# Kernel optimization log

Measured on AMD Instinct MI355X. Metric: run time of the kernel, lower is better.

## Reference

```python
import jax, jax.numpy as jnp
import numpy as np

V, D, T_MAX, H, L = 32000, 1024, 1024, 16, 8
HD = D // H
DFF = 4 * D
EPS = 1e-5


def _pos_encoding(T, d_model, dtype=jnp.float32):
    pos = jnp.arange(T, dtype=jnp.float32)[:, None]                      # [T,1]
    div = jnp.exp(jnp.arange(0, d_model, 2, dtype=jnp.float32) * (-jnp.log(10000.0) / d_model))
    pe = jnp.zeros((T, d_model), dtype=jnp.float32)
    pe = pe.at[:, 0::2].set(jnp.sin(pos * div))
    pe = pe.at[:, 1::2].set(jnp.cos(pos * div))
    return pe.astype(dtype)


def _layernorm(x, g, b):
    mu = jnp.mean(x, axis=-1, keepdims=True)
    var = jnp.mean(jnp.square(x - mu), axis=-1, keepdims=True)
    return (x - mu) * jax.lax.rsqrt(var + EPS) * g + b


def setup_inputs() -> dict:
    key = jax.random.key(0)
    ks = jax.random.split(key, 9)
    s = 0.02
    return {
        "idx": jax.random.randint(ks[0], (2, 1024), 0, V),
        "embed": jax.random.normal(ks[1], (V, D), jnp.float32) * s,
        "Wqkv": jax.random.normal(ks[2], (L, D, 3 * D), jnp.float32) * s,
        "Wproj": jax.random.normal(ks[3], (L, D, D), jnp.float32) * s,
        "bproj": jnp.zeros((L, D), jnp.float32),
        "ln1_g": jnp.ones((L, D), jnp.float32),
        "ln1_b": jnp.zeros((L, D), jnp.float32),
        "ln2_g": jnp.ones((L, D), jnp.float32),
        "ln2_b": jnp.zeros((L, D), jnp.float32),
        "W1": jax.random.normal(ks[4], (L, D, DFF), jnp.float32) * s,
        "b1": jnp.zeros((L, DFF), jnp.float32),
        "W2": jax.random.normal(ks[5], (L, DFF, D), jnp.float32) * s,
        "b2": jnp.zeros((L, D), jnp.float32),
        "lnf_g": jnp.ones((D,), jnp.float32),
        "lnf_b": jnp.zeros((D,), jnp.float32),
        "Whead": jax.random.normal(ks[6], (D, V), jnp.float32) * s,
    }


def _attn(x, Wqkv, Wproj, bproj):
    B, T, C = x.shape
    qkv = (x @ Wqkv).reshape(B, T, 3, H, HD)
    q, k, v = [jnp.transpose(qkv[:, :, i], (0, 2, 1, 3)) for i in range(3)]  # [B,H,T,HD]
    scores = jnp.einsum('bhqd,bhkd->bhqk', q, k) * (HD ** -0.5)
    mask = jnp.tril(jnp.ones((T, T), dtype=bool))
    scores = jnp.where(mask, scores, -jnp.inf)
    w = jax.nn.softmax(scores, axis=-1)
    out = jnp.einsum('bhqk,bhkd->bhqd', w, v)
    out = jnp.transpose(out, (0, 2, 1, 3)).reshape(B, T, C)
    return out @ Wproj + bproj


def reference(idx, embed, Wqkv, Wproj, bproj, ln1_g, ln1_b, ln2_g, ln2_b,
              W1, b1, W2, b2, lnf_g, lnf_b, Whead):
    idx = idx[:, :T_MAX]
    T = idx.shape[1]
    x = embed[idx] + _pos_encoding(T, D)[None]          # [B,T,D]
    for l in range(L):
        x = x + _attn(_layernorm(x, ln1_g[l], ln1_b[l]), Wqkv[l], Wproj[l], bproj[l])
        h = _layernorm(x, ln2_g[l], ln2_b[l])
        x = x + jax.nn.relu(h @ W1[l] + b1[l]) @ W2[l] + b2[l]
    x = _layernorm(x, lnf_g, lnf_b)
    return x @ Whead                                     # [B,T,V]
```

## Files before the change

### kernel.cpp

```cpp
#include <hip/hip_runtime.h>
#include <cstddef>

#define DM    1024
#define TSEQ  1024
#define NB    2
#define NHEAD 16
#define HDIM  64
#define NLAYER 8
#define DFFN  4096
#define NVOC  32000
#define NROWS (NB*TSEQ)

typedef __attribute__((ext_vector_type(8))) short short8;
typedef __attribute__((ext_vector_type(4))) float f32x4;

static __device__ __forceinline__ unsigned short f2bf(float f) {
    union { float f; unsigned int u; } v; v.f = f;
    unsigned int r = v.u + 0x7FFF + ((v.u >> 16) & 1);
    return (unsigned short)(r >> 16);
}

static __device__ __forceinline__ void gload_lds16(const void* g, void* l) {
    __builtin_amdgcn_global_load_lds(
        (const __attribute__((address_space(1))) unsigned int*)g,
        (__attribute__((address_space(3))) unsigned int*)l, 16, 0, 0);
}

__global__ __launch_bounds__(256)
void embed_pos_k(const int* __restrict__ idx, const float* __restrict__ embed,
                 float* __restrict__ x)
{
    int row = blockIdx.x;
    int t   = row & (TSEQ - 1);
    int tid = threadIdx.x;
    int token = idx[row];
    const float* er = embed + (size_t)token * DM;
    float* xr = x + (size_t)row * DM;
    const float neg_ln1e4_over_d = -9.210340371976184f / (float)DM;
    for (int i = tid; i < DM; i += 256) {
        int half = i >> 1;
        float div = expf((float)(2 * half) * neg_ln1e4_over_d);
        float ang = (float)t * div;
        float pe = (i & 1) ? cosf(ang) : sinf(ang);
        xr[i] = er[i] + pe;
    }
}

__global__ __launch_bounds__(256)
void layernorm_k(const float* __restrict__ x, const float* __restrict__ g,
                 const float* __restrict__ b, unsigned short* __restrict__ y)
{
    int row = blockIdx.x;
    int tid = threadIdx.x;
    const float* xr = x + (size_t)row * DM;
    unsigned short* yr = y + (size_t)row * DM;
    float vals[4];
    float s = 0.f;
    #pragma unroll
    for (int i = 0; i < 4; ++i) { vals[i] = xr[tid + 256 * i]; s += vals[i]; }
    __shared__ float red[256];
    red[tid] = s; __syncthreads();
    for (int st = 128; st > 0; st >>= 1) {
        if (tid < st) red[tid] += red[tid + st];
        __syncthreads();
    }
    float mu = red[0] * (1.f / DM);
    __syncthreads();
    float v = 0.f;
    #pragma unroll
    for (int i = 0; i < 4; ++i) { float d = vals[i] - mu; v += d * d; }
    red[tid] = v; __syncthreads();
    for (int st = 128; st > 0; st >>= 1) {
        if (tid < st) red[tid] += red[tid + st];
        __syncthreads();
    }
    float rstd = rsqrtf(red[0] * (1.f / DM) + 1e-5f);
    #pragma unroll
    for (int i = 0; i < 4; ++i) {
        int c = tid + 256 * i;
        yr[c] = f2bf((vals[i] - mu) * rstd * g[c] + b[c]);
    }
}

__global__ __launch_bounds__(256)
void convt_k(const float* __restrict__ src, unsigned short* __restrict__ dst,
             int K, int N)
{
    __shared__ __align__(16) unsigned short T[64][72];
    const int tid = threadIdx.x;
    const int n0 = blockIdx.x * 64, k0 = blockIdx.y * 64;
    const float* s = src + (size_t)blockIdx.z * K * N;
    unsigned short* d = dst + (size_t)blockIdx.z * K * N;
    #pragma unroll
    for (int q = 0; q < 4; ++q) {
        int f4 = tid + q * 256;
        int kk = f4 >> 4, nn = (f4 & 15) * 4;
        float4 v = *(const float4*)(s + (size_t)(k0 + kk) * N + n0 + nn);
        int swz = ((nn >> 2) & 7) << 3;
        T[nn + 0][kk ^ swz] = f2bf(v.x);
        T[nn + 1][kk ^ swz] = f2bf(v.y);
        T[nn + 2][kk ^ swz] = f2bf(v.z);
        T[nn + 3][kk ^ swz] = f2bf(v.w);
    }
    __syncthreads();
    #pragma unroll
    for (int q = 0; q < 2; ++q) {
        int s8 = tid + q * 256;
        int nn = s8 >> 3, kc = (s8 & 7) * 8;
        int swz = ((nn >> 2) & 7) << 3;
        *(short8*)(d + (size_t)(n0 + nn) * K + k0 + kc) =
            *(const short8*)&T[nn][kc ^ swz];
    }
}

template<int BM, bool OUT_BF16>
__global__ __launch_bounds__(256)
void gemm_tn(const unsigned short* __restrict__ A, const unsigned short* __restrict__ BT,
             const float* __restrict__ bias, const float* __restrict__ residual,
             void* __restrict__ Cout, int M, int N, int K, int KS, int relu)
{
    constexpr int FR = BM / 32;
    constexpr int RPW = BM / 4;
    constexpr int NI = BM / 64;
    __shared__ __align__(16) unsigned short As[2][BM][32];
    __shared__ __align__(16) unsigned short Bs[2][BM][32];

    const int tid = threadIdx.x;
    const int lane = tid & 63;
    const int w = tid >> 6;
    const int wr = w >> 1, wc = w & 1;
    const int l16 = lane & 15, g = lane >> 4;

    const int nby = M / BM;
    const int nwg = (N / BM) * nby;
    const int cpx = nwg >> 3;
    const int bid = blockIdx.x;
    const int sbid = (bid & 7) * cpx + (bid >> 3);
    const int row0 = (sbid % nby) * BM;
    const int col0 = (sbid / nby) * BM;

    const int srow = w * RPW + (lane >> 2);
    const int scol = (lane & 3) * 8;

    const unsigned short* ga = A  + (size_t)(row0 + srow) * KS + (size_t)blockIdx.y * K + scol;
    const unsigned short* gb = BT + (size_t)(col0 + srow) * KS + (size_t)blockIdx.y * K + scol;

    f32x4 acc[FR][FR] = {};

    #pragma unroll
    for (int i = 0; i < NI; ++i) {
        gload_lds16(ga + (size_t)(i * 16) * KS, &As[0][srow + i * 16][scol]);
        gload_lds16(gb + (size_t)(i * 16) * KS, &Bs[0][srow + i * 16][scol]);
    }
    __syncthreads();

    int cur = 0;
    for (int k0 = 0; k0 < K; k0 += 32) {
        if (k0 + 32 < K) {
            #pragma unroll
            for (int i = 0; i < NI; ++i) {
                gload_lds16(ga + k0 + 32 + (size_t)(i * 16) * KS, &As[cur ^ 1][srow + i * 16][scol]);
                gload_lds16(gb + k0 + 32 + (size_t)(i * 16) * KS, &Bs[cur ^ 1][srow + i * 16][scol]);
            }
        }
        short8 af[FR], bf[FR];
        #pragma unroll
        for (int i = 0; i < FR; ++i)
            af[i] = *(const short8*)&As[cur][wr * (BM / 2) + i * 16 + l16][g * 8];
        #pragma unroll
        for (int j = 0; j < FR; ++j)
            bf[j] = *(const short8*)&Bs[cur][wc * (BM / 2) + j * 16 + l16][g * 8];
        #pragma unroll
        for (int i = 0; i < FR; ++i)
            #pragma unroll
            for (int j = 0; j < FR; ++j)
                acc[i][j] = __builtin_amdgcn_mfma_f32_16x16x32_bf16(af[i], bf[j], acc[i][j], 0, 0, 0);
        __syncthreads();
        cur ^= 1;
    }

    float* Cf = (float*)Cout + (size_t)blockIdx.y * M * N;
    #pragma unroll
    for (int i = 0; i < FR; ++i) {
        #pragma unroll
        for (int j = 0; j < FR; ++j) {
            #pragma unroll
            for (int r = 0; r < 4; ++r) {
                int row = row0 + wr * (BM / 2) + i * 16 + g * 4 + r;
                int col = col0 + wc * (BM / 2) + j * 16 + l16;
                float v = acc[i][j][r];
                if (bias)     v += bias[col];
                if (residual) v += residual[(size_t)row * N + col];
                if (relu)     v = fmaxf(v, 0.f);
                if (OUT_BF16) ((unsigned short*)Cout)[(size_t)row * N + col] = f2bf(v);
                else          Cf[(size_t)row * N + col] = v;
            }
        }
    }
}

__global__ __launch_bounds__(256)
void reduce_sk(const float* __restrict__ P, int nsplit, const float* __restrict__ bias,
               const float* __restrict__ Xres, float* __restrict__ X, int Ncols)
{
    const size_t i4 = (size_t)blockIdx.x * 256 + threadIdx.x;
    const int col4 = (int)(i4 & (Ncols / 4 - 1)) * 4;
    float4 v = *(const float4*)(Xres + i4 * 4);
    float4 bb = *(const float4*)(bias + col4);
    v.x += bb.x; v.y += bb.y; v.z += bb.z; v.w += bb.w;
    const size_t tot4 = (size_t)NROWS * Ncols / 4;
    for (int s = 0; s < nsplit; ++s) {
        float4 p = *(const float4*)(P + (s * tot4 + i4) * 4);
        v.x += p.x; v.y += p.y; v.z += p.z; v.w += p.w;
    }
    *(float4*)(X + i4 * 4) = v;
}

__global__ __launch_bounds__(256)
void attn_flash_k(const unsigned short* __restrict__ qkv, unsigned short* __restrict__ out)
{
    __shared__ unsigned short Ks[64][72];
    __shared__ unsigned short Vt[64][72];
    __shared__ unsigned short Ps[4][16][72];

    const int tid = threadIdx.x;
    const int lane = tid & 63;
    const int w = tid >> 6;
    const int l16 = lane & 15, g = lane >> 4;
    const int h = blockIdx.y;
    const int b = blockIdx.z;

    const size_t rstr = 3 * DM;
    const unsigned short* base = qkv + (size_t)b * TSEQ * rstr + h * HDIM;

    const int krow0 = tid >> 3, kcol = (tid & 7) * 8;
    const int vkv = tid & 63, vdg = tid >> 6;

    short8 kreg0, kreg1, vreg0, vreg1;

    #pragma unroll
    for (int pass = 0; pass < 2; ++pass) {
        const int qb = pass ? (15 - (int)blockIdx.x) : (int)blockIdx.x;
        const int q0 = qb * 64;
        const int nt = qb + 1;

        const int qrow_w = q0 + w * 16 + l16;
        short8 aq0 = *(const short8*)(base + (size_t)qrow_w * rstr + g * 8);
        short8 aq1 = *(const short8*)(base + (size_t)qrow_w * rstr + 32 + g * 8);

        f32x4 acc_o[4] = {};
        float m_r[4] = {-INFINITY, -INFINITY, -INFINITY, -INFINITY};
        float l_r[4] = {};

        {
            const unsigned short* kb = base + DM;
            kreg0 = *(const short8*)(kb + (size_t)krow0 * rstr + kcol);
            kreg1 = *(const short8*)(kb + (size_t)(32 + krow0) * rstr + kcol);
            const unsigned short* vsrc = base + (size_t)vkv * rstr + 2 * DM + vdg * 16;
            vreg0 = *(const short8*)vsrc;
            vreg1 = *(const short8*)(vsrc + 8);
        }

        for (int t = 0; t < nt; ++t) {
            *(short8*)&Ks[krow0][kcol] = kreg0;
            *(short8*)&Ks[32 + krow0][kcol] = kreg1;
            #pragma unroll
            for (int j = 0; j < 8; ++j) Vt[vdg * 16 + j][vkv] = (unsigned short)vreg0[j];
            #pragma unroll
            for (int j = 0; j < 8; ++j) Vt[vdg * 16 + 8 + j][vkv] = (unsigned short)vreg1[j];
            __syncthreads();

            if (t + 1 < nt) {
                const int kv0 = (t + 1) * 64;
                const unsigned short* kb = base + (size_t)kv0 * rstr + DM;
                kreg0 = *(const short8*)(kb + (size_t)krow0 * rstr + kcol);
                kreg1 = *(const short8*)(kb + (size_t)(32 + krow0) * rstr + kcol);
                const unsigned short* vsrc = base + (size_t)(kv0 + vkv) * rstr + 2 * DM + vdg * 16;
                vreg0 = *(const short8*)vsrc;
                vreg1 = *(const short8*)(vsrc + 8);
            }

            const int kv0 = t * 64;
            f32x4 acc_s[4] = {};
            #pragma unroll
            for (int ks = 0; ks < 4; ++ks) {
                short8 bk0 = *(const short8*)&Ks[ks * 16 + l16][g * 8];
                short8 bk1 = *(const short8*)&Ks[ks * 16 + l16][32 + g * 8];
                acc_s[ks] = __builtin_amdgcn_mfma_f32_16x16x32_bf16(aq0, bk0, acc_s[ks], 0, 0, 0);
                acc_s[ks] = __builtin_amdgcn_mfma_f32_16x16x32_bf16(aq1, bk1, acc_s[ks], 0, 0, 0);
            }
            const bool need_mask = (kv0 + 63 > q0 + w * 16);
            float alpha[4];
            #pragma unroll
            for (int r = 0; r < 4; ++r) {
                const int q_abs = q0 + w * 16 + g * 4 + r;
                float s[4];
                #pragma unroll
                for (int ks = 0; ks < 4; ++ks) {
                    s[ks] = acc_s[ks][r] * 0.125f;
                    if (need_mask && (kv0 + ks * 16 + l16 > q_abs)) s[ks] = -INFINITY;
                }
                float pm = fmaxf(fmaxf(s[0], s[1]), fmaxf(s[2], s[3]));
                #pragma unroll
                for (int msk = 1; msk <= 8; msk <<= 1)
                    pm = fmaxf(pm, __shfl_xor(pm, msk));
                float mnew = fmaxf(m_r[r], pm);
                alpha[r] = __expf(m_r[r] - mnew);
                m_r[r] = mnew;
                float p[4], psum = 0.f;
                #pragma unroll
                for (int ks = 0; ks < 4; ++ks) {
                    p[ks] = (s[ks] == -INFINITY) ? 0.f : __expf(s[ks] - mnew);
                    psum += p[ks];
                }
                #pragma unroll
                for (int msk = 1; msk <= 8; msk <<= 1)
                    psum += __shfl_xor(psum, msk);
                l_r[r] = l_r[r] * alpha[r] + psum;
                #pragma unroll
                for (int ks = 0; ks < 4; ++ks)
                    Ps[w][g * 4 + r][ks * 16 + l16] = f2bf(p[ks]);
            }
            #pragma unroll
            for (int ds = 0; ds < 4; ++ds)
                #pragma unroll
                for (int r = 0; r < 4; ++r)
                    acc_o[ds][r] *= alpha[r];
            short8 ap0 = *(const short8*)&Ps[w][l16][g * 8];
            short8 ap1 = *(const short8*)&Ps[w][l16][32 + g * 8];
            #pragma unroll
            for (int ds = 0; ds < 4; ++ds) {
                short8 bv0 = *(const short8*)&Vt[ds * 16 + l16][g * 8];
                short8 bv1 = *(const short8*)&Vt[ds * 16 + l16][32 + g * 8];
                acc_o[ds] = __builtin_amdgcn_mfma_f32_16x16x32_bf16(ap0, bv0, acc_o[ds], 0, 0, 0);
                acc_o[ds] = __builtin_amdgcn_mfma_f32_16x16x32_bf16(ap1, bv1, acc_o[ds], 0, 0, 0);
            }
            __syncthreads();
        }

        #pragma unroll
        for (int ds = 0; ds < 4; ++ds)
            #pragma unroll
            for (int r = 0; r < 4; ++r) {
                int row = q0 + w * 16 + g * 4 + r;
                out[((size_t)b * TSEQ + row) * DM + h * HDIM + ds * 16 + l16] =
                    f2bf(acc_o[ds][r] * (1.f / l_r[r]));
            }
    }
}

extern "C" void kernel_launch(void* const* d_in, const int* in_sizes, int n_in,
                              void* d_out, int out_size, void* d_ws, size_t ws_size,
                              hipStream_t stream)
{
    const int*   idx    = (const int*)  d_in[0];
    const float* embed  = (const float*)d_in[1];
    const float* Wqkv   = (const float*)d_in[2];
    const float* Wproj  = (const float*)d_in[3];
    const float* bproj  = (const float*)d_in[4];
    const float* ln1_g  = (const float*)d_in[5];
    const float* ln1_b  = (const float*)d_in[6];
    const float* ln2_g  = (const float*)d_in[7];
    const float* ln2_b  = (const float*)d_in[8];
    const float* W1     = (const float*)d_in[9];
    const float* b1     = (const float*)d_in[10];
    const float* W2     = (const float*)d_in[11];
    const float* b2     = (const float*)d_in[12];
    const float* lnf_g  = (const float*)d_in[13];
    const float* lnf_b  = (const float*)d_in[14];
    const float* Whead  = (const float*)d_in[15];
    float* out = (float*)d_out;

    float* X = (float*)d_ws;
    float* PK = X + (size_t)NROWS * DM;
    unsigned short* u = (unsigned short*)(PK + (size_t)4 * NROWS * DM);
    unsigned short* XN     = u;  u += (size_t)NROWS * DM;
    unsigned short* QKVb   = u;  u += (size_t)NROWS * 3 * DM;
    unsigned short* ATT    = u;  u += (size_t)NROWS * DM;
    unsigned short* FFH    = u;  u += (size_t)NROWS * DFFN;
    unsigned short* WqkvT  = u;  u += (size_t)NLAYER * 3 * DM * DM;
    unsigned short* WprojT = u;  u += (size_t)NLAYER * DM * DM;
    unsigned short* W1T    = u;  u += (size_t)NLAYER * DFFN * DM;
    unsigned short* W2T    = u;  u += (size_t)NLAYER * DM * DFFN;
    unsigned short* WheadT = u;  u += (size_t)NVOC * DM;

    convt_k<<<dim3(3 * DM / 64, DM / 64, NLAYER), 256, 0, stream>>>(Wqkv,  WqkvT,  DM,   3 * DM);
    convt_k<<<dim3(DM / 64,     DM / 64, NLAYER), 256, 0, stream>>>(Wproj, WprojT, DM,   DM);
    convt_k<<<dim3(DFFN / 64,   DM / 64, NLAYER), 256, 0, stream>>>(W1,    W1T,    DM,   DFFN);
    convt_k<<<dim3(DM / 64,   DFFN / 64, NLAYER), 256, 0, stream>>>(W2,    W2T,    DFFN, DM);
    convt_k<<<dim3(NVOC / 64,   DM / 64, 1),      256, 0, stream>>>(Whead, WheadT, DM,   NVOC);

    embed_pos_k<<<NROWS, 256, 0, stream>>>(idx, embed, X);

    const int nred = (NROWS * DM / 4) / 256;

    for (int l = 0; l < NLAYER; ++l) {
        const unsigned short* wqkvT_l  = WqkvT  + (size_t)l * 3 * DM * DM;
        const unsigned short* wprojT_l = WprojT + (size_t)l * DM * DM;
        const unsigned short* w1T_l    = W1T    + (size_t)l * DFFN * DM;
        const unsigned short* w2T_l    = W2T    + (size_t)l * DM * DFFN;
        const float* bproj_l = bproj + (size_t)l * DM;
        const float* b1_l = b1 + (size_t)l * DFFN;
        const float* b2_l = b2 + (size_t)l * DM;

        layernorm_k<<<NROWS, 256, 0, stream>>>(X, ln1_g + (size_t)l * DM,
                                               ln1_b + (size_t)l * DM, XN);
        {
            int nwg = (NROWS / 128) * (3 * DM / 128);
            gemm_tn<128, true><<<nwg, 256, 0, stream>>>(XN, wqkvT_l, nullptr, nullptr,
                                                        QKVb, NROWS, 3 * DM, DM, DM, 0);
        }
        {
            dim3 grid(TSEQ / 128, NHEAD, NB);
            attn_flash_k<<<grid, 256, 0, stream>>>(QKVb, ATT);
        }
        {
            dim3 grid((NROWS / 128) * (DM / 128), 2);
            gemm_tn<128, false><<<grid, 256, 0, stream>>>(ATT, wprojT_l, nullptr, nullptr,
                                                          PK, NROWS, DM, 512, DM, 0);
            reduce_sk<<<nred, 256, 0, stream>>>(PK, 2, bproj_l, X, X, DM);
        }
        layernorm_k<<<NROWS, 256, 0, stream>>>(X, ln2_g + (size_t)l * DM,
                                               ln2_b + (size_t)l * DM, XN);
        {
            int nwg = (NROWS / 128) * (DFFN / 128);
            gemm_tn<128, true><<<nwg, 256, 0, stream>>>(XN, w1T_l, b1_l, nullptr,
                                                        FFH, NROWS, DFFN, DM, DM, 1);
        }
        {
            dim3 grid((NROWS / 128) * (DM / 128), 4);
            gemm_tn<128, false><<<grid, 256, 0, stream>>>(FFH, w2T_l, nullptr, nullptr,
                                                          PK, NROWS, DM, 1024, DFFN, 0);
            reduce_sk<<<nred, 256, 0, stream>>>(PK, 4, b2_l, X, X, DM);
        }
    }

    layernorm_k<<<NROWS, 256, 0, stream>>>(X, lnf_g, lnf_b, XN);
    {
        int nwg = (NROWS / 128) * (NVOC / 128);
        gemm_tn<128, false><<<nwg, 256, 0, stream>>>(XN, WheadT, nullptr, nullptr,
                                                     out, NROWS, NVOC, DM, DM, 0);
    }
}
```

Before: 1.905 ms.

## Fuse split-K reduction with layernorm and swizzle GEMM LDS layout

Replaces the separate split-K reduce and layernorm kernels with one row-wise kernel. It sums the partials, adds the bias and residual, writes X, then computes the next layernorm into the bf16 buffer. This removes a kernel launch and a full re-read of X per residual step. It also XOR-swizzles the GEMM LDS column slots, on both the global-to-LDS writes and the fragment reads, to reduce bank conflicts. The risk is a wrong swizzle mapping between the write and read sides.

```diff
diff --git a/kernel.cpp b/kernel.cpp
--- a/kernel.cpp
+++ b/kernel.cpp
@@ -83,6 +83,52 @@
 }
 
 __global__ __launch_bounds__(256)
+void reduce_ln_k(const float* __restrict__ P, int nsplit, const float* __restrict__ bias,
+                 float* __restrict__ X, const float* __restrict__ g,
+                 const float* __restrict__ b, unsigned short* __restrict__ XN)
+{
+    const int row = blockIdx.x;
+    const int tid = threadIdx.x;
+    const size_t off4 = (size_t)row * 256 + tid;
+    const size_t tot4 = (size_t)NROWS * 256;
+
+    float4 v = *((const float4*)X + off4);
+    float4 bb = *((const float4*)bias + tid);
+    v.x += bb.x; v.y += bb.y; v.z += bb.z; v.w += bb.w;
+    for (int s = 0; s < nsplit; ++s) {
+        float4 p = *((const float4*)P + s * tot4 + off4);
+        v.x += p.x; v.y += p.y; v.z += p.z; v.w += p.w;
+    }
+    *((float4*)X + off4) = v;
+
+    __shared__ float red[256];
+    red[tid] = v.x + v.y + v.z + v.w;
+    __syncthreads();
+    for (int st = 128; st > 0; st >>= 1) {
+        if (tid < st) red[tid] += red[tid + st];
+        __syncthreads();
+    }
+    float mu = red[0] * (1.f / DM);
+    __syncthreads();
+    float4 d = make_float4(v.x - mu, v.y - mu, v.z - mu, v.w - mu);
+    red[tid] = d.x * d.x + d.y * d.y + d.z * d.z + d.w * d.w;
+    __syncthreads();
+    for (int st = 128; st > 0; st >>= 1) {
+        if (tid < st) red[tid] += red[tid + st];
+        __syncthreads();
+    }
+    float rstd = rsqrtf(red[0] * (1.f / DM) + 1e-5f);
+    float4 gg = *((const float4*)g + tid);
+    float4 bbn = *((const float4*)b + tid);
+    unsigned short o[4];
+    o[0] = f2bf(d.x * rstd * gg.x + bbn.x);
+    o[1] = f2bf(d.y * rstd * gg.y + bbn.y);
+    o[2] = f2bf(d.z * rstd * gg.z + bbn.z);
+    o[3] = f2bf(d.w * rstd * gg.w + bbn.w);
+    *(ushort4*)(XN + (size_t)row * DM + tid * 4) = *(ushort4*)o;
+}
+
+__global__ __launch_bounds__(256)
 void convt_k(const float* __restrict__ src, unsigned short* __restrict__ dst,
              int K, int N)
 {
@@ -140,7 +186,8 @@
     const int col0 = (sbid / nby) * BM;
 
     const int srow = w * RPW + (lane >> 2);
-    const int scol = (lane & 3) * 8;
+    const int scol = (((lane & 3) ^ ((lane >> 3) & 3)) << 3);
+    const int rslot = ((g ^ ((l16 >> 1) & 3)) << 3);
 
     const unsigned short* ga = A  + (size_t)(row0 + srow) * KS + (size_t)blockIdx.y * K + scol;
     const unsigned short* gb = BT + (size_t)(col0 + srow) * KS + (size_t)blockIdx.y * K + scol;
@@ -149,8 +196,8 @@
 
     #pragma unroll
     for (int i = 0; i < NI; ++i) {
-        gload_lds16(ga + (size_t)(i * 16) * KS, &As[0][srow + i * 16][scol]);
-        gload_lds16(gb + (size_t)(i * 16) * KS, &Bs[0][srow + i * 16][scol]);
+        gload_lds16(ga + (size_t)(i * 16) * KS, &As[0][srow + i * 16][(lane & 3) << 3]);
+        gload_lds16(gb + (size_t)(i * 16) * KS, &Bs[0][srow + i * 16][(lane & 3) << 3]);
     }
     __syncthreads();
 
@@ -159,17 +206,17 @@
         if (k0 + 32 < K) {
             #pragma unroll
             for (int i = 0; i < NI; ++i) {
-                gload_lds16(ga + k0 + 32 + (size_t)(i * 16) * KS, &As[cur ^ 1][srow + i * 16][scol]);
-                gload_lds16(gb + k0 + 32 + (size_t)(i * 16) * KS, &Bs[cur ^ 1][srow + i * 16][scol]);
+                gload_lds16(ga + k0 + 32 + (size_t)(i * 16) * KS, &As[cur ^ 1][srow + i * 16][(lane & 3) << 3]);
+                gload_lds16(gb + k0 + 32 + (size_t)(i * 16) * KS, &Bs[cur ^ 1][srow + i * 16][(lane & 3) << 3]);
             }
         }
         short8 af[FR], bf[FR];
         #pragma unroll
         for (int i = 0; i < FR; ++i)
-            af[i] = *(const short8*)&As[cur][wr * (BM / 2) + i * 16 + l16][g * 8];
+            af[i] = *(const short8*)&As[cur][wr * (BM / 2) + i * 16 + l16][rslot];
         #pragma unroll
         for (int j = 0; j < FR; ++j)
-            bf[j] = *(const short8*)&Bs[cur][wc * (BM / 2) + j * 16 + l16][g * 8];
+            bf[j] = *(const short8*)&Bs[cur][wc * (BM / 2) + j * 16 + l16][rslot];
         #pragma unroll
         for (int i = 0; i < FR; ++i)
             #pragma unroll
@@ -200,23 +247,6 @@
 }
 
 __global__ __launch_bounds__(256)
-void reduce_sk(const float* __restrict__ P, int nsplit, const float* __restrict__ bias,
-               const float* __restrict__ Xres, float* __restrict__ X, int Ncols)
-{
-    const size_t i4 = (size_t)blockIdx.x * 256 + threadIdx.x;
-    const int col4 = (int)(i4 & (Ncols / 4 - 1)) * 4;
-    float4 v = *(const float4*)(Xres + i4 * 4);
-    float4 bb = *(const float4*)(bias + col4);
-    v.x += bb.x; v.y += bb.y; v.z += bb.z; v.w += bb.w;
-    const size_t tot4 = (size_t)NROWS * Ncols / 4;
-    for (int s = 0; s < nsplit; ++s) {
-        float4 p = *(const float4*)(P + (s * tot4 + i4) * 4);
-        v.x += p.x; v.y += p.y; v.z += p.z; v.w += p.w;
-    }
-    *(float4*)(X + i4 * 4) = v;
-}
-
-__global__ __launch_bounds__(256)
 void attn_flash_k(const unsigned short* __restrict__ qkv, unsigned short* __restrict__ out)
 {
     __shared__ unsigned short Ks[64][72];
@@ -271,11 +301,11 @@
             __syncthreads();
 
             if (t + 1 < nt) {
-                const int kv0 = (t + 1) * 64;
-                const unsigned short* kb = base + (size_t)kv0 * rstr + DM;
+                const int kv0n = (t + 1) * 64;
+                const unsigned short* kb = base + (size_t)kv0n * rstr + DM;
                 kreg0 = *(const short8*)(kb + (size_t)krow0 * rstr + kcol);
                 kreg1 = *(const short8*)(kb + (size_t)(32 + krow0) * rstr + kcol);
-                const unsigned short* vsrc = base + (size_t)(kv0 + vkv) * rstr + 2 * DM + vdg * 16;
+                const unsigned short* vsrc = base + (size_t)(kv0n + vkv) * rstr + 2 * DM + vdg * 16;
                 vreg0 = *(const short8*)vsrc;
                 vreg1 = *(const short8*)(vsrc + 8);
             }
@@ -391,8 +421,7 @@
     convt_k<<<dim3(NVOC / 64,   DM / 64, 1),      256, 0, stream>>>(Whead, WheadT, DM,   NVOC);
 
     embed_pos_k<<<NROWS, 256, 0, stream>>>(idx, embed, X);
-
-    const int nred = (NROWS * DM / 4) / 256;
+    layernorm_k<<<NROWS, 256, 0, stream>>>(X, ln1_g, ln1_b, XN);
 
     for (int l = 0; l < NLAYER; ++l) {
         const unsigned short* wqkvT_l  = WqkvT  + (size_t)l * 3 * DM * DM;
@@ -403,8 +432,6 @@
         const float* b1_l = b1 + (size_t)l * DFFN;
         const float* b2_l = b2 + (size_t)l * DM;
 
-        layernorm_k<<<NROWS, 256, 0, stream>>>(X, ln1_g + (size_t)l * DM,
-                                               ln1_b + (size_t)l * DM, XN);
         {
             int nwg = (NROWS / 128) * (3 * DM / 128);
             gemm_tn<128, true><<<nwg, 256, 0, stream>>>(XN, wqkvT_l, nullptr, nullptr,
@@ -418,10 +445,10 @@
             dim3 grid((NROWS / 128) * (DM / 128), 2);
             gemm_tn<128, false><<<grid, 256, 0, stream>>>(ATT, wprojT_l, nullptr, nullptr,
                                                           PK, NROWS, DM, 512, DM, 0);
-            reduce_sk<<<nred, 256, 0, stream>>>(PK, 2, bproj_l, X, X, DM);
-        }
-        layernorm_k<<<NROWS, 256, 0, stream>>>(X, ln2_g + (size_t)l * DM,
-                                               ln2_b + (size_t)l * DM, XN);
+            reduce_ln_k<<<NROWS, 256, 0, stream>>>(PK, 2, bproj_l, X,
+                                                   ln2_g + (size_t)l * DM,
+                                                   ln2_b + (size_t)l * DM, XN);
+        }
         {
             int nwg = (NROWS / 128) * (DFFN / 128);
             gemm_tn<128, true><<<nwg, 256, 0, stream>>>(XN, w1T_l, b1_l, nullptr,
@@ -431,11 +458,12 @@
             dim3 grid((NROWS / 128) * (DM / 128), 4);
             gemm_tn<128, false><<<grid, 256, 0, stream>>>(FFH, w2T_l, nullptr, nullptr,
                                                           PK, NROWS, DM, 1024, DFFN, 0);
-            reduce_sk<<<nred, 256, 0, stream>>>(PK, 4, b2_l, X, X, DM);
-        }
-    }
-
-    layernorm_k<<<NROWS, 256, 0, stream>>>(X, lnf_g, lnf_b, XN);
+            const float* ng = (l + 1 < NLAYER) ? ln1_g + (size_t)(l + 1) * DM : lnf_g;
+            const float* nb = (l + 1 < NLAYER) ? ln1_b + (size_t)(l + 1) * DM : lnf_b;
+            reduce_ln_k<<<NROWS, 256, 0, stream>>>(PK, 4, b2_l, X, ng, nb, XN);
+        }
+    }
+
     {
         int nwg = (NROWS / 128) * (NVOC / 128);
         gemm_tn<128, false><<<nwg, 256, 0, stream>>>(XN, WheadT, nullptr, nullptr,
```

New measurement: 1.846 ms. 3.1% less time.
